# Performance work log

Hardware: AMD Instinct MI355X
Metric: run time of the kernel (lower is better)

## Reference

```python
import jax, jax.numpy as jnp
import numpy as np

LN_EPS = 1e-5


def setup_inputs() -> dict:
    key = jax.random.key(0)
    ks = jax.random.split(key, 8)
    N, H, E, D, B = 262144, 768, 768, 2048, 65536
    return {
        "u_t": jax.random.normal(ks[0], (B, E), dtype=jnp.float32),
        "s_i": jax.random.randint(ks[1], (B,), 0, N, dtype=jnp.int64),
        "speaker_embeddings": jax.random.normal(ks[2], (N, H), dtype=jnp.float32),
        "W1": jax.random.normal(ks[3], (D, H + E), dtype=jnp.float32) * 0.02,
        "b1": jax.random.normal(ks[4], (D,), dtype=jnp.float32) * 0.02,
        "W2": jax.random.normal(ks[5], (H, D), dtype=jnp.float32) * 0.02,
        "b2": jax.random.normal(ks[6], (H,), dtype=jnp.float32) * 0.02,
        "ln_gamma": jnp.ones((H,), dtype=jnp.float32),
        "ln_beta": jnp.zeros((H,), dtype=jnp.float32),
    }


def reference(u_t, s_i, speaker_embeddings, W1, b1, W2, b2, ln_gamma, ln_beta):
    # gather speaker vectors: [B, H]
    h_t = speaker_embeddings[s_i]
    # concat [u_t, h_t] along features: [B, E+H]
    x = jnp.concatenate([u_t, h_t], axis=-1)
    # Linear -> GELU (exact, torch default) -> (Dropout=identity in eval)
    h = jax.nn.gelu(jnp.einsum("bf,df->bd", x, W1) + b1, approximate=False)
    # Linear -> (Dropout=identity) : [B, H]
    y = jnp.einsum("bd,hd->bh", h, W2) + b2
    # LayerNorm over last dim
    mu = jnp.mean(y, axis=-1, keepdims=True)
    var = jnp.mean((y - mu) ** 2, axis=-1, keepdims=True)
    new_h_t = (y - mu) * jax.lax.rsqrt(var + LN_EPS) * ln_gamma + ln_beta
    # scatter-add back into the memory table (duplicates accumulate)
    updated = speaker_embeddings.at[s_i].add(new_h_t)
    return new_h_t, updated
```

## Files before the change

### kernel.cpp

```cpp
#include <hip/hip_runtime.h>
#include <hip/hip_bf16.h>

typedef unsigned short u16;
typedef unsigned int u32;
typedef short bf16x8 __attribute__((ext_vector_type(8)));
typedef float f32x4 __attribute__((ext_vector_type(4)));

#define BAR() asm volatile("s_barrier" ::: "memory")
#define WAITV4() asm volatile("s_waitcnt vmcnt(4)" ::: "memory")
#define WAITV0() asm volatile("s_waitcnt vmcnt(0)" ::: "memory")
#define WAITL() asm volatile("s_waitcnt lgkmcnt(0)" ::: "memory")

__device__ __forceinline__ unsigned pk2(float lo, float hi) {
    unsigned a = (unsigned)__builtin_bit_cast(u16, __float2bfloat16(lo));
    unsigned b = (unsigned)__builtin_bit_cast(u16, __float2bfloat16(hi));
    return a | (b << 16);
}
__device__ __forceinline__ u16 f2bf(float v) {
    return __builtin_bit_cast(u16, __float2bfloat16(v));
}
__device__ __forceinline__ void gl_lds16(const u16* g, u16* l) {
    __builtin_amdgcn_global_load_lds(
        (const __attribute__((address_space(1))) u32*)g,
        (__attribute__((address_space(3))) u32*)l, 16, 0, 0);
}

__global__ void cvtbf(const float4* __restrict__ s, uint2* __restrict__ d, int n4) {
    int i = blockIdx.x * blockDim.x + threadIdx.x;
    int stride = gridDim.x * blockDim.x;
    for (; i < n4; i += stride) {
        float4 f = s[i];
        uint2 o;
        o.x = pk2(f.x, f.y);
        o.y = pk2(f.z, f.w);
        d[i] = o;
    }
}

__global__ __launch_bounds__(256) void xbuild(const float* __restrict__ u_t,
                                              const float* __restrict__ emb,
                                              const int* __restrict__ s_i,
                                              u16* __restrict__ xb) {
    const long u = (long)blockIdx.x * blockDim.x + threadIdx.x;
    const int row = (int)(u / 192);
    const int c8 = (int)(u % 192);
    const float* src = (c8 < 96) ? (u_t + (long)row * 768 + c8 * 8)
                                 : (emb + (long)s_i[row] * 768 + (c8 - 96) * 8);
    float4 f0 = ((const float4*)src)[0];
    float4 f1 = ((const float4*)src)[1];
    uint4 o;
    o.x = pk2(f0.x, f0.y);
    o.y = pk2(f0.z, f0.w);
    o.z = pk2(f1.x, f1.y);
    o.w = pk2(f1.z, f1.w);
    *(uint4*)(xb + u * 8) = o;
}

template <int LDK, int NT, int TN, int EPI>
__global__ __launch_bounds__(512, 2) void gemm256(
    const u16* __restrict__ Ag, const u16* __restrict__ Bg,
    const float* __restrict__ bias, u16* __restrict__ outb,
    float* __restrict__ outf) {
    __shared__ __align__(16) u16 lds[65536];

    const int tid = threadIdx.x;
    const int lane = tid & 63;
    const int wv = tid >> 6;
    const int wm = wv >> 2;
    const int wn = wv & 3;

    const int cpx = (int)gridDim.x >> 3;
    const int tile = ((int)blockIdx.x & 7) * cpx + ((int)blockIdx.x >> 3);
    const int tm = tile / TN, tn = tile % TN;
    const long rowBase = (long)tm * 256;
    const long colBase = (long)tn * 256;

    const int srow = tid >> 2;
    const int gch = (tid & 3) ^ ((tid >> 3) & 3);
    const u16* pA = Ag + (rowBase + srow) * (long)LDK + gch * 8;
    const u16* pB = Bg + (colBase + srow) * (long)LDK + gch * 8;
    const int dstBase = wv * 512;

    auto stageA = [&](int kt, int ks, int b) {
        const u16* s = pA + kt * 64 + ks * 32;
        u16* d = lds + b * 32768 + ks * 8192 + dstBase;
        gl_lds16(s, d);
        gl_lds16(s + (long)128 * LDK, d + 4096);
    };
    auto stageB = [&](int kt, int ks, int b) {
        const u16* s = pB + kt * 64 + ks * 32;
        u16* d = lds + b * 32768 + 16384 + ks * 8192 + dstBase;
        gl_lds16(s, d);
        gl_lds16(s + (long)128 * LDK, d + 4096);
    };

    const int l15 = lane & 15, lc = lane >> 4;
    int offA[8], offB[4];
#pragma unroll
    for (int i = 0; i < 8; ++i) {
        int r = wm * 128 + i * 16 + l15;
        offA[i] = r * 32 + ((lc ^ ((r >> 1) & 3)) << 3);
    }
#pragma unroll
    for (int n = 0; n < 4; ++n) {
        int r = wn * 64 + n * 16 + l15;
        offB[n] = r * 32 + ((lc ^ ((r >> 1) & 3)) << 3);
    }

    f32x4 acc[8][4];
    const f32x4 zero = {0.f, 0.f, 0.f, 0.f};
#pragma unroll
    for (int m = 0; m < 8; ++m)
#pragma unroll
        for (int n = 0; n < 4; ++n) acc[m][n] = zero;

    stageA(0, 0, 0);
    stageB(0, 0, 0);
    stageA(0, 1, 0);
    stageB(0, 1, 0);
    WAITV4();
    BAR();

    bf16x8 bA[4], bB[4];
    for (int kt = 0; kt < NT; ++kt) {
        const int b = kt & 1;
        const u16* rA0 = lds + b * 32768;
        const u16* rB0 = rA0 + 16384;
        const u16* rA1 = rA0 + 8192;
        const u16* rB1 = rB0 + 8192;
        const bool pf = (kt + 1 < NT);

#pragma unroll
        for (int n = 0; n < 4; ++n) bB[n] = *(const bf16x8*)(rB0 + offB[n]);
#pragma unroll
        for (int m = 0; m < 4; ++m) bA[m] = *(const bf16x8*)(rA0 + offA[m]);
        if (pf) stageA(kt + 1, 0, b ^ 1);
        BAR();
        WAITL();
        __builtin_amdgcn_s_setprio(1);
#pragma unroll
        for (int m = 0; m < 4; ++m)
#pragma unroll
            for (int n = 0; n < 4; ++n)
                acc[m][n] = __builtin_amdgcn_mfma_f32_16x16x32_bf16(bA[m], bB[n], acc[m][n], 0, 0, 0);
        __builtin_amdgcn_s_setprio(0);
        BAR();

#pragma unroll
        for (int m = 0; m < 4; ++m) bA[m] = *(const bf16x8*)(rA0 + offA[4 + m]);
        if (pf) stageB(kt + 1, 0, b ^ 1);
        BAR();
        WAITL();
        __builtin_amdgcn_s_setprio(1);
#pragma unroll
        for (int m = 0; m < 4; ++m)
#pragma unroll
            for (int n = 0; n < 4; ++n)
                acc[4 + m][n] = __builtin_amdgcn_mfma_f32_16x16x32_bf16(bA[m], bB[n], acc[4 + m][n], 0, 0, 0);
        __builtin_amdgcn_s_setprio(0);
        if (pf) { WAITV4(); } else { WAITV0(); }
        BAR();

#pragma unroll
        for (int n = 0; n < 4; ++n) bB[n] = *(const bf16x8*)(rB1 + offB[n]);
#pragma unroll
        for (int m = 0; m < 4; ++m) bA[m] = *(const bf16x8*)(rA1 + offA[m]);
        if (pf) stageA(kt + 1, 1, b ^ 1);
        BAR();
        WAITL();
        __builtin_amdgcn_s_setprio(1);
#pragma unroll
        for (int m = 0; m < 4; ++m)
#pragma unroll
            for (int n = 0; n < 4; ++n)
                acc[m][n] = __builtin_amdgcn_mfma_f32_16x16x32_bf16(bA[m], bB[n], acc[m][n], 0, 0, 0);
        __builtin_amdgcn_s_setprio(0);
        BAR();

#pragma unroll
        for (int m = 0; m < 4; ++m) bA[m] = *(const bf16x8*)(rA1 + offA[4 + m]);
        if (pf) stageB(kt + 1, 1, b ^ 1);
        BAR();
        WAITL();
        __builtin_amdgcn_s_setprio(1);
#pragma unroll
        for (int m = 0; m < 4; ++m)
#pragma unroll
            for (int n = 0; n < 4; ++n)
                acc[4 + m][n] = __builtin_amdgcn_mfma_f32_16x16x32_bf16(bA[m], bB[n], acc[4 + m][n], 0, 0, 0);
        __builtin_amdgcn_s_setprio(0);
        if (pf) { WAITV4(); } else { WAITV0(); }
        BAR();
    }

    const int N = TN * 256;
#pragma unroll
    for (int n = 0; n < 4; ++n) {
        long gc = colBase + wn * 64 + n * 16 + l15;
        float bv = bias[gc];
#pragma unroll
        for (int i = 0; i < 8; ++i) {
            long gr = rowBase + wm * 128 + i * 16 + (lc << 2);
#pragma unroll
            for (int j = 0; j < 4; ++j) {
                float v = acc[i][n][j] + bv;
                if constexpr (EPI == 0) {
                    float w = v * v;
                    float z = v * fmaf(w, -0.0713548162f, -1.5957691216f);
                    v = __fdividef(v, 1.0f + __expf(z));
                    outb[(gr + j) * N + gc] = f2bf(v);
                } else {
                    outf[(gr + j) * N + gc] = v;
                }
            }
        }
    }
}

__global__ __launch_bounds__(256) void ln_scatter(float* __restrict__ y,
                                                  const float* __restrict__ gamma,
                                                  const float* __restrict__ beta,
                                                  const int* __restrict__ s_i,
                                                  float* __restrict__ upd) {
    const int lane = threadIdx.x & 63;
    const long row = (long)blockIdx.x * 4 + (threadIdx.x >> 6);
    const long base = row * 768;
    float v[12];
#pragma unroll
    for (int i = 0; i < 12; ++i) v[i] = y[base + i * 64 + lane];
    float s = 0.f, q = 0.f;
#pragma unroll
    for (int i = 0; i < 12; ++i) { s += v[i]; q += v[i] * v[i]; }
#pragma unroll
    for (int off = 32; off > 0; off >>= 1) {
        s += __shfl_xor(s, off, 64);
        q += __shfl_xor(q, off, 64);
    }
    const float mu = s * (1.f / 768.f);
    const float var = q * (1.f / 768.f) - mu * mu;
    const float inv = rsqrtf(var + 1e-5f);
    const long si = s_i[row];
#pragma unroll
    for (int i = 0; i < 12; ++i) {
        int c = i * 64 + lane;
        float r = (v[i] - mu) * inv * gamma[c] + beta[c];
        y[base + c] = r;
        atomicAdd(&upd[si * 768 + c], r);
    }
}

__global__ void copy4(const float4* __restrict__ s, float4* __restrict__ d, long n) {
    long i = (long)blockIdx.x * blockDim.x + threadIdx.x;
    long stride = (long)gridDim.x * blockDim.x;
    for (; i < n; i += stride) d[i] = s[i];
}

extern "C" void kernel_launch(void* const* d_in, const int* in_sizes, int n_in,
                              void* d_out, int out_size, void* d_ws, size_t ws_size,
                              hipStream_t stream) {
    const float* u_t = (const float*)d_in[0];
    const int* s_i = (const int*)d_in[1];
    const float* emb = (const float*)d_in[2];
    const float* W1 = (const float*)d_in[3];
    const float* b1 = (const float*)d_in[4];
    const float* W2 = (const float*)d_in[5];
    const float* b2 = (const float*)d_in[6];
    const float* gamma = (const float*)d_in[7];
    const float* beta = (const float*)d_in[8];

    float* out = (float*)d_out;
    float* newh = out;
    float* upd = out + 50331648L;

    u16* base = (u16*)upd;
    u16* xb = base;
    u16* w1b = base + 100663296L;
    u16* hbuf = base + 103809024L;
    u16* w2b = base + 238026752L;

    cvtbf<<<1024, 256, 0, stream>>>((const float4*)W1, (uint2*)w1b, 786432);
    cvtbf<<<1024, 256, 0, stream>>>((const float4*)W2, (uint2*)w2b, 393216);
    xbuild<<<49152, 256, 0, stream>>>(u_t, emb, s_i, xb);
    gemm256<1536, 24, 8, 0><<<2048, 512, 0, stream>>>(xb, w1b, b1, hbuf, nullptr);
    gemm256<2048, 32, 3, 1><<<768, 512, 0, stream>>>(hbuf, w2b, b2, nullptr, newh);
    copy4<<<2048, 256, 0, stream>>>((const float4*)emb, (float4*)upd, 50331648L);
    ln_scatter<<<16384, 256, 0, stream>>>(newh, gamma, beta, s_i, upd);
}
```

Baseline: 1.326 ms.

## Restructure GEMM k-loop into two phases with split LDS waits

The four-stage inner k-loop becomes two phases per k-tile. Each phase loads B and both halves of A from LDS up front, issues the A and B prefetches together, and waits with lgkmcnt(4) so the first 16 MFMAs start while the second A half is still arriving. Scheduling barriers keep the compiler from reordering this. The change halves the number of block barriers per tile and relaxes launch bounds to one block per CU, which allows more registers for the extra fragments but may lower occupancy.

```diff
diff --git a/kernel.cpp b/kernel.cpp
--- a/kernel.cpp
+++ b/kernel.cpp
@@ -9,7 +9,9 @@
 #define BAR() asm volatile("s_barrier" ::: "memory")
 #define WAITV4() asm volatile("s_waitcnt vmcnt(4)" ::: "memory")
 #define WAITV0() asm volatile("s_waitcnt vmcnt(0)" ::: "memory")
+#define WAITL4() asm volatile("s_waitcnt lgkmcnt(4)" ::: "memory")
 #define WAITL() asm volatile("s_waitcnt lgkmcnt(0)" ::: "memory")
+#define SCHED() __builtin_amdgcn_sched_barrier(0)
 
 __device__ __forceinline__ unsigned pk2(float lo, float hi) {
     unsigned a = (unsigned)__builtin_bit_cast(u16, __float2bfloat16(lo));
@@ -57,7 +59,7 @@
 }
 
 template <int LDK, int NT, int TN, int EPI>
-__global__ __launch_bounds__(512, 2) void gemm256(
+__global__ __launch_bounds__(512, 1) void gemm256(
     const u16* __restrict__ Ag, const u16* __restrict__ Bg,
     const float* __restrict__ bias, u16* __restrict__ outb,
     float* __restrict__ outf) {
@@ -121,76 +123,47 @@
     WAITV4();
     BAR();
 
-    bf16x8 bA[4], bB[4];
     for (int kt = 0; kt < NT; ++kt) {
         const int b = kt & 1;
-        const u16* rA0 = lds + b * 32768;
-        const u16* rB0 = rA0 + 16384;
-        const u16* rA1 = rA0 + 8192;
-        const u16* rB1 = rB0 + 8192;
+        const u16* base = lds + b * 32768;
         const bool pf = (kt + 1 < NT);
 
 #pragma unroll
-        for (int n = 0; n < 4; ++n) bB[n] = *(const bf16x8*)(rB0 + offB[n]);
-#pragma unroll
-        for (int m = 0; m < 4; ++m) bA[m] = *(const bf16x8*)(rA0 + offA[m]);
-        if (pf) stageA(kt + 1, 0, b ^ 1);
-        BAR();
-        WAITL();
-        __builtin_amdgcn_s_setprio(1);
-#pragma unroll
-        for (int m = 0; m < 4; ++m)
-#pragma unroll
-            for (int n = 0; n < 4; ++n)
-                acc[m][n] = __builtin_amdgcn_mfma_f32_16x16x32_bf16(bA[m], bB[n], acc[m][n], 0, 0, 0);
-        __builtin_amdgcn_s_setprio(0);
-        BAR();
-
-#pragma unroll
-        for (int m = 0; m < 4; ++m) bA[m] = *(const bf16x8*)(rA0 + offA[4 + m]);
-        if (pf) stageB(kt + 1, 0, b ^ 1);
-        BAR();
-        WAITL();
-        __builtin_amdgcn_s_setprio(1);
-#pragma unroll
-        for (int m = 0; m < 4; ++m)
-#pragma unroll
-            for (int n = 0; n < 4; ++n)
-                acc[4 + m][n] = __builtin_amdgcn_mfma_f32_16x16x32_bf16(bA[m], bB[n], acc[4 + m][n], 0, 0, 0);
-        __builtin_amdgcn_s_setprio(0);
-        if (pf) { WAITV4(); } else { WAITV0(); }
-        BAR();
-
-#pragma unroll
-        for (int n = 0; n < 4; ++n) bB[n] = *(const bf16x8*)(rB1 + offB[n]);
-#pragma unroll
-        for (int m = 0; m < 4; ++m) bA[m] = *(const bf16x8*)(rA1 + offA[m]);
-        if (pf) stageA(kt + 1, 1, b ^ 1);
-        BAR();
-        WAITL();
-        __builtin_amdgcn_s_setprio(1);
-#pragma unroll
-        for (int m = 0; m < 4; ++m)
-#pragma unroll
-            for (int n = 0; n < 4; ++n)
-                acc[m][n] = __builtin_amdgcn_mfma_f32_16x16x32_bf16(bA[m], bB[n], acc[m][n], 0, 0, 0);
-        __builtin_amdgcn_s_setprio(0);
-        BAR();
-
-#pragma unroll
-        for (int m = 0; m < 4; ++m) bA[m] = *(const bf16x8*)(rA1 + offA[4 + m]);
-        if (pf) stageB(kt + 1, 1, b ^ 1);
-        BAR();
-        WAITL();
-        __builtin_amdgcn_s_setprio(1);
-#pragma unroll
-        for (int m = 0; m < 4; ++m)
-#pragma unroll
-            for (int n = 0; n < 4; ++n)
-                acc[4 + m][n] = __builtin_amdgcn_mfma_f32_16x16x32_bf16(bA[m], bB[n], acc[4 + m][n], 0, 0, 0);
-        __builtin_amdgcn_s_setprio(0);
-        if (pf) { WAITV4(); } else { WAITV0(); }
-        BAR();
+        for (int ph = 0; ph < 2; ++ph) {
+            const u16* rA = base + ph * 8192;
+            const u16* rB = base + 16384 + ph * 8192;
+            bf16x8 xB[4], xA0[4], xA1[4];
+#pragma unroll
+            for (int n = 0; n < 4; ++n) xB[n] = *(const bf16x8*)(rB + offB[n]);
+            SCHED();
+#pragma unroll
+            for (int m = 0; m < 4; ++m) xA0[m] = *(const bf16x8*)(rA + offA[m]);
+            SCHED();
+#pragma unroll
+            for (int m = 0; m < 4; ++m) xA1[m] = *(const bf16x8*)(rA + offA[4 + m]);
+            SCHED();
+            if (pf) { stageA(kt + 1, ph, b ^ 1); stageB(kt + 1, ph, b ^ 1); }
+            BAR();
+            WAITL4();
+            SCHED();
+            __builtin_amdgcn_s_setprio(1);
+#pragma unroll
+            for (int m = 0; m < 4; ++m)
+#pragma unroll
+                for (int n = 0; n < 4; ++n)
+                    acc[m][n] = __builtin_amdgcn_mfma_f32_16x16x32_bf16(xA0[m], xB[n], acc[m][n], 0, 0, 0);
+            SCHED();
+            WAITL();
+            SCHED();
+#pragma unroll
+            for (int m = 0; m < 4; ++m)
+#pragma unroll
+                for (int n = 0; n < 4; ++n)
+                    acc[4 + m][n] = __builtin_amdgcn_mfma_f32_16x16x32_bf16(xA1[m], xB[n], acc[4 + m][n], 0, 0, 0);
+            __builtin_amdgcn_s_setprio(0);
+            if (pf) { WAITV4(); } else { WAITV0(); }
+            BAR();
+        }
     }
 
     const int N = TN * 256;
```

Measured after the change: 1.369 ms. 3.3% more time.

## Fuse second GEMM with LayerNorm using full-row 64x768 tiles

Applied to the files above, without the earlier changes.

Replaces the 256x256-tiled second GEMM and the separate LayerNorm pass with a kernel that computes whole 64-row by 768-column output tiles. Row statistics are reduced in-block through shuffles and shared memory, and normalized values are written directly. The aim is to avoid writing and re-reading un-normalized y. The trade-off is a simpler, non-pipelined main loop with a barrier per k-step, no double buffering, and B re-reads of the full W2 per block, so GEMM efficiency may drop.

```diff
diff --git a/kernel.cpp b/kernel.cpp
--- a/kernel.cpp
+++ b/kernel.cpp
@@ -56,11 +56,10 @@
     *(uint4*)(xb + u * 8) = o;
 }
 
-template <int LDK, int NT, int TN, int EPI>
+template <int LDK, int NT, int TN>
 __global__ __launch_bounds__(512, 2) void gemm256(
     const u16* __restrict__ Ag, const u16* __restrict__ Bg,
-    const float* __restrict__ bias, u16* __restrict__ outb,
-    float* __restrict__ outf) {
+    const float* __restrict__ bias, u16* __restrict__ outb) {
     __shared__ __align__(16) u16 lds[65536];
 
     const int tid = threadIdx.x;
@@ -204,48 +203,158 @@
 #pragma unroll
             for (int j = 0; j < 4; ++j) {
                 float v = acc[i][n][j] + bv;
-                if constexpr (EPI == 0) {
-                    float w = v * v;
-                    float z = v * fmaf(w, -0.0713548162f, -1.5957691216f);
-                    v = __fdividef(v, 1.0f + __expf(z));
-                    outb[(gr + j) * N + gc] = f2bf(v);
-                } else {
-                    outf[(gr + j) * N + gc] = v;
-                }
-            }
-        }
-    }
-}
-
-__global__ __launch_bounds__(256) void ln_scatter(float* __restrict__ y,
-                                                  const float* __restrict__ gamma,
-                                                  const float* __restrict__ beta,
-                                                  const int* __restrict__ s_i,
-                                                  float* __restrict__ upd) {
+                float w = v * v;
+                float z = v * fmaf(w, -0.0713548162f, -1.5957691216f);
+                v = __fdividef(v, 1.0f + __expf(z));
+                outb[(gr + j) * N + gc] = f2bf(v);
+            }
+        }
+    }
+}
+
+__global__ __launch_bounds__(512, 2) void gemm2ln(
+    const u16* __restrict__ hbuf, const u16* __restrict__ w2b,
+    const float* __restrict__ b2, const float* __restrict__ gamma,
+    const float* __restrict__ beta, float* __restrict__ newh) {
+    __shared__ __align__(16) u16 As[4096];
+    __shared__ __align__(16) u16 Bs[49152];
+    __shared__ float redS[8][64];
+    __shared__ float redQ[8][64];
+    __shared__ float lnMu[64];
+    __shared__ float lnInv[64];
+
+    const int tid = threadIdx.x;
+    const int lane = tid & 63;
+    const int wv = tid >> 6;
+    const int l15 = lane & 15, lc = lane >> 4;
+    const long rowBase = (long)blockIdx.x * 64;
+
+    const int srow = tid >> 3;
+    const int sch = (tid & 7) ^ (srow & 7);
+    const u16* srcA = hbuf + (rowBase + srow) * 2048 + sch * 8;
+    const u16* srcB = w2b + (long)srow * 2048 + sch * 8;
+
+    int offA[2][4], offB[2][6];
+#pragma unroll
+    for (int kk = 0; kk < 2; ++kk) {
+#pragma unroll
+        for (int i = 0; i < 4; ++i) {
+            int r = i * 16 + l15;
+            offA[kk][i] = r * 64 + (((kk * 4 + lc) ^ (r & 7)) << 3);
+        }
+#pragma unroll
+        for (int n = 0; n < 6; ++n) {
+            int r = wv * 96 + n * 16 + l15;
+            offB[kk][n] = r * 64 + (((kk * 4 + lc) ^ (r & 7)) << 3);
+        }
+    }
+
+    f32x4 acc[4][6];
+    const f32x4 zero = {0.f, 0.f, 0.f, 0.f};
+#pragma unroll
+    for (int i = 0; i < 4; ++i)
+#pragma unroll
+        for (int n = 0; n < 6; ++n) acc[i][n] = zero;
+
+    for (int kt = 0; kt < 32; ++kt) {
+        gl_lds16(srcA + kt * 64, As + wv * 512);
+#pragma unroll
+        for (int p = 0; p < 12; ++p)
+            gl_lds16(srcB + (long)p * 131072 + kt * 64, Bs + p * 4096 + wv * 512);
+        __syncthreads();
+#pragma unroll
+        for (int kk = 0; kk < 2; ++kk) {
+            bf16x8 aF[4], bF[6];
+#pragma unroll
+            for (int i = 0; i < 4; ++i) aF[i] = *(const bf16x8*)(As + offA[kk][i]);
+#pragma unroll
+            for (int n = 0; n < 6; ++n) bF[n] = *(const bf16x8*)(Bs + offB[kk][n]);
+#pragma unroll
+            for (int i = 0; i < 4; ++i)
+#pragma unroll
+                for (int n = 0; n < 6; ++n)
+                    acc[i][n] = __builtin_amdgcn_mfma_f32_16x16x32_bf16(aF[i], bF[n], acc[i][n], 0, 0, 0);
+        }
+        __syncthreads();
+    }
+
+    float bv[6];
+#pragma unroll
+    for (int n = 0; n < 6; ++n) bv[n] = b2[wv * 96 + n * 16 + l15];
+
+    float ps[4][4], pq[4][4];
+#pragma unroll
+    for (int i = 0; i < 4; ++i)
+#pragma unroll
+        for (int j = 0; j < 4; ++j) {
+            float s = 0.f, q = 0.f;
+#pragma unroll
+            for (int n = 0; n < 6; ++n) {
+                float v = acc[i][n][j] + bv[n];
+                s += v;
+                q += v * v;
+            }
+            ps[i][j] = s;
+            pq[i][j] = q;
+        }
+#pragma unroll
+    for (int off = 1; off < 16; off <<= 1) {
+#pragma unroll
+        for (int i = 0; i < 4; ++i)
+#pragma unroll
+            for (int j = 0; j < 4; ++j) {
+                ps[i][j] += __shfl_xor(ps[i][j], off, 64);
+                pq[i][j] += __shfl_xor(pq[i][j], off, 64);
+            }
+    }
+    if (l15 == 0) {
+#pragma unroll
+        for (int i = 0; i < 4; ++i)
+#pragma unroll
+            for (int j = 0; j < 4; ++j) {
+                int r = i * 16 + lc * 4 + j;
+                redS[wv][r] = ps[i][j];
+                redQ[wv][r] = pq[i][j];
+            }
+    }
+    __syncthreads();
+    if (tid < 64) {
+        float s = 0.f, q = 0.f;
+#pragma unroll
+        for (int w = 0; w < 8; ++w) { s += redS[w][tid]; q += redQ[w][tid]; }
+        float mu = s * (1.f / 768.f);
+        float var = q * (1.f / 768.f) - mu * mu;
+        lnMu[tid] = mu;
+        lnInv[tid] = rsqrtf(var + 1e-5f);
+    }
+    __syncthreads();
+
+#pragma unroll
+    for (int n = 0; n < 6; ++n) {
+        int col = wv * 96 + n * 16 + l15;
+        float g = gamma[col], bt = beta[col];
+#pragma unroll
+        for (int i = 0; i < 4; ++i) {
+#pragma unroll
+            for (int j = 0; j < 4; ++j) {
+                int r = i * 16 + lc * 4 + j;
+                float v = acc[i][n][j] + bv[n];
+                newh[(rowBase + r) * 768 + col] = (v - lnMu[r]) * lnInv[r] * g + bt;
+            }
+        }
+    }
+}
+
+__global__ __launch_bounds__(256) void scatter_add(const float* __restrict__ newh,
+                                                   const int* __restrict__ s_i,
+                                                   float* __restrict__ upd) {
     const int lane = threadIdx.x & 63;
-    const long row = (long)blockIdx.x * 4 + (threadIdx.x >> 6);
-    const long base = row * 768;
-    float v[12];
-#pragma unroll
-    for (int i = 0; i < 12; ++i) v[i] = y[base + i * 64 + lane];
-    float s = 0.f, q = 0.f;
-#pragma unroll
-    for (int i = 0; i < 12; ++i) { s += v[i]; q += v[i] * v[i]; }
-#pragma unroll
-    for (int off = 32; off > 0; off >>= 1) {
-        s += __shfl_xor(s, off, 64);
-        q += __shfl_xor(q, off, 64);
-    }
-    const float mu = s * (1.f / 768.f);
-    const float var = q * (1.f / 768.f) - mu * mu;
-    const float inv = rsqrtf(var + 1e-5f);
-    const long si = s_i[row];
+    const long b = (long)blockIdx.x * 4 + (threadIdx.x >> 6);
+    const long s = s_i[b];
 #pragma unroll
     for (int i = 0; i < 12; ++i) {
         int c = i * 64 + lane;
-        float r = (v[i] - mu) * inv * gamma[c] + beta[c];
-        y[base + c] = r;
-        atomicAdd(&upd[si * 768 + c], r);
+        atomicAdd(&upd[s * 768 + c], newh[b * 768 + c]);
     }
 }
 
@@ -281,8 +390,8 @@
     cvtbf<<<1024, 256, 0, stream>>>((const float4*)W1, (uint2*)w1b, 786432);
     cvtbf<<<1024, 256, 0, stream>>>((const float4*)W2, (uint2*)w2b, 393216);
     xbuild<<<49152, 256, 0, stream>>>(u_t, emb, s_i, xb);
-    gemm256<1536, 24, 8, 0><<<2048, 512, 0, stream>>>(xb, w1b, b1, hbuf, nullptr);
-    gemm256<2048, 32, 3, 1><<<768, 512, 0, stream>>>(hbuf, w2b, b2, nullptr, newh);
+    gemm256<1536, 24, 8><<<2048, 512, 0, stream>>>(xb, w1b, b1, hbuf);
+    gemm2ln<<<1024, 512, 0, stream>>>(hbuf, w2b, b2, gamma, beta, newh);
     copy4<<<2048, 256, 0, stream>>>((const float4*)emb, (float4*)upd, 50331648L);
-    ln_scatter<<<16384, 256, 0, stream>>>(newh, gamma, beta, s_i, upd);
-}
+    scatter_add<<<16384, 256, 0, stream>>>(newh, s_i, upd);
+}
```

After: 1.428 ms. 1.08x slower.

## Deepen GEMM prefetch pipeline by unrolling two k-tiles per loop iteration

Applied to the files above, without the earlier changes.

Restructures the bf16 MFMA GEMM main loop to process two k-tiles per iteration with fixed LDS buffer pointers. It prefetches an extra half-tile in the prologue so global-to-LDS loads run further ahead of the MFMA consumption. The aim is to hide more global load latency and drop per-iteration buffer index arithmetic. The cost is larger code and an implicit assumption that NT is even; the vmcnt wait thresholds were left unchanged despite more loads in flight.

```diff
diff --git a/kernel.cpp b/kernel.cpp
--- a/kernel.cpp
+++ b/kernel.cpp
@@ -118,23 +118,32 @@
     stageB(0, 0, 0);
     stageA(0, 1, 0);
     stageB(0, 1, 0);
+    stageA(1, 0, 1);
+    stageB(1, 0, 1);
     WAITV4();
     BAR();
 
+    const u16* rA0k0 = lds;
+    const u16* rA0k1 = lds + 8192;
+    const u16* rB0k0 = lds + 16384;
+    const u16* rB0k1 = lds + 24576;
+    const u16* rA1k0 = lds + 32768;
+    const u16* rA1k1 = lds + 40960;
+    const u16* rB1k0 = lds + 49152;
+    const u16* rB1k1 = lds + 57344;
+
     bf16x8 bA[4], bB[4];
-    for (int kt = 0; kt < NT; ++kt) {
-        const int b = kt & 1;
-        const u16* rA0 = lds + b * 32768;
-        const u16* rB0 = rA0 + 16384;
-        const u16* rA1 = rA0 + 8192;
-        const u16* rB1 = rB0 + 8192;
-        const bool pf = (kt + 1 < NT);
-
-#pragma unroll
-        for (int n = 0; n < 4; ++n) bB[n] = *(const bf16x8*)(rB0 + offB[n]);
-#pragma unroll
-        for (int m = 0; m < 4; ++m) bA[m] = *(const bf16x8*)(rA0 + offA[m]);
-        if (pf) stageA(kt + 1, 0, b ^ 1);
+    const int NT2 = NT / 2;
+    for (int tp = 0; tp < NT2; ++tp) {
+        const int t1 = 2 * tp + 1;
+        const int t2 = 2 * tp + 2;
+        const bool pf = (t2 < NT);
+
+#pragma unroll
+        for (int n = 0; n < 4; ++n) bB[n] = *(const bf16x8*)(rB0k0 + offB[n]);
+#pragma unroll
+        for (int m = 0; m < 4; ++m) bA[m] = *(const bf16x8*)(rA0k0 + offA[m]);
+        stageA(t1, 1, 1);
         BAR();
         WAITL();
         __builtin_amdgcn_s_setprio(1);
@@ -147,8 +156,8 @@
         BAR();
 
 #pragma unroll
-        for (int m = 0; m < 4; ++m) bA[m] = *(const bf16x8*)(rA0 + offA[4 + m]);
-        if (pf) stageB(kt + 1, 0, b ^ 1);
+        for (int m = 0; m < 4; ++m) bA[m] = *(const bf16x8*)(rA0k0 + offA[4 + m]);
+        stageB(t1, 1, 1);
         BAR();
         WAITL();
         __builtin_amdgcn_s_setprio(1);
@@ -158,14 +167,44 @@
             for (int n = 0; n < 4; ++n)
                 acc[4 + m][n] = __builtin_amdgcn_mfma_f32_16x16x32_bf16(bA[m], bB[n], acc[4 + m][n], 0, 0, 0);
         __builtin_amdgcn_s_setprio(0);
+        BAR();
+
+#pragma unroll
+        for (int n = 0; n < 4; ++n) bB[n] = *(const bf16x8*)(rB0k1 + offB[n]);
+#pragma unroll
+        for (int m = 0; m < 4; ++m) bA[m] = *(const bf16x8*)(rA0k1 + offA[m]);
+        if (pf) stageA(t2, 0, 0);
+        BAR();
+        WAITL();
+        __builtin_amdgcn_s_setprio(1);
+#pragma unroll
+        for (int m = 0; m < 4; ++m)
+#pragma unroll
+            for (int n = 0; n < 4; ++n)
+                acc[m][n] = __builtin_amdgcn_mfma_f32_16x16x32_bf16(bA[m], bB[n], acc[m][n], 0, 0, 0);
+        __builtin_amdgcn_s_setprio(0);
+        BAR();
+
+#pragma unroll
+        for (int m = 0; m < 4; ++m) bA[m] = *(const bf16x8*)(rA0k1 + offA[4 + m]);
+        if (pf) stageB(t2, 0, 0);
+        BAR();
+        WAITL();
+        __builtin_amdgcn_s_setprio(1);
+#pragma unroll
+        for (int m = 0; m < 4; ++m)
+#pragma unroll
+            for (int n = 0; n < 4; ++n)
+                acc[4 + m][n] = __builtin_amdgcn_mfma_f32_16x16x32_bf16(bA[m], bB[n], acc[4 + m][n], 0, 0, 0);
+        __builtin_amdgcn_s_setprio(0);
         if (pf) { WAITV4(); } else { WAITV0(); }
         BAR();
 
 #pragma unroll
-        for (int n = 0; n < 4; ++n) bB[n] = *(const bf16x8*)(rB1 + offB[n]);
-#pragma unroll
-        for (int m = 0; m < 4; ++m) bA[m] = *(const bf16x8*)(rA1 + offA[m]);
-        if (pf) stageA(kt + 1, 1, b ^ 1);
+        for (int n = 0; n < 4; ++n) bB[n] = *(const bf16x8*)(rB1k0 + offB[n]);
+#pragma unroll
+        for (int m = 0; m < 4; ++m) bA[m] = *(const bf16x8*)(rA1k0 + offA[m]);
+        if (pf) stageA(t2, 1, 0);
         BAR();
         WAITL();
         __builtin_amdgcn_s_setprio(1);
@@ -178,8 +217,38 @@
         BAR();
 
 #pragma unroll
-        for (int m = 0; m < 4; ++m) bA[m] = *(const bf16x8*)(rA1 + offA[4 + m]);
-        if (pf) stageB(kt + 1, 1, b ^ 1);
+        for (int m = 0; m < 4; ++m) bA[m] = *(const bf16x8*)(rA1k0 + offA[4 + m]);
+        if (pf) stageB(t2, 1, 0);
+        BAR();
+        WAITL();
+        __builtin_amdgcn_s_setprio(1);
+#pragma unroll
+        for (int m = 0; m < 4; ++m)
+#pragma unroll
+            for (int n = 0; n < 4; ++n)
+                acc[4 + m][n] = __builtin_amdgcn_mfma_f32_16x16x32_bf16(bA[m], bB[n], acc[4 + m][n], 0, 0, 0);
+        __builtin_amdgcn_s_setprio(0);
+        BAR();
+
+#pragma unroll
+        for (int n = 0; n < 4; ++n) bB[n] = *(const bf16x8*)(rB1k1 + offB[n]);
+#pragma unroll
+        for (int m = 0; m < 4; ++m) bA[m] = *(const bf16x8*)(rA1k1 + offA[m]);
+        if (pf) stageA(t2 + 1, 0, 1);
+        BAR();
+        WAITL();
+        __builtin_amdgcn_s_setprio(1);
+#pragma unroll
+        for (int m = 0; m < 4; ++m)
+#pragma unroll
+            for (int n = 0; n < 4; ++n)
+                acc[m][n] = __builtin_amdgcn_mfma_f32_16x16x32_bf16(bA[m], bB[n], acc[m][n], 0, 0, 0);
+        __builtin_amdgcn_s_setprio(0);
+        BAR();
+
+#pragma unroll
+        for (int m = 0; m < 4; ++m) bA[m] = *(const bf16x8*)(rA1k1 + offA[4 + m]);
+        if (pf) stageB(t2 + 1, 0, 1);
         BAR();
         WAITL();
         __builtin_amdgcn_s_setprio(1);
```

New measurement: 1.327 ms. Within noise of the previous version (+0.1%).
